# Optimization experiments

Measured on AMD Instinct MI355X. Metric: run time of the kernel, lower is better.

The kernel has to match this reference:

```python
import jax, jax.numpy as jnp
import numpy as np

N_HEADS = 16

def setup_inputs() -> dict:
    key = jax.random.key(0)
    ks = jax.random.split(key, 7)
    B, S, D = 2, 2048, 1024
    sc = 1.0 / np.sqrt(D)
    return {
        "x": jax.random.normal(ks[0], (B, S, D), dtype=jnp.float32),
        "Wq": jax.random.normal(ks[1], (D, D), dtype=jnp.float32) * sc,
        "bq": jax.random.normal(ks[2], (D,), dtype=jnp.float32) * 0.02,
        "Wk": jax.random.normal(ks[3], (D, D), dtype=jnp.float32) * sc,
        "bk": jax.random.normal(ks[4], (D,), dtype=jnp.float32) * 0.02,
        "Wv": jax.random.normal(ks[5], (D, D), dtype=jnp.float32) * sc,
        "bv": jax.random.normal(ks[6], (D,), dtype=jnp.float32) * 0.02,
    }

def reference(x, Wq, bq, Wk, bk, Wv, bv):
    B, S, D = x.shape
    H = N_HEADS
    W = D // H  # head width
    # QKV projections (torch Linear: x @ W^T + b); here weights stored as [D_in, D_out]
    q = x @ Wq + bq
    k = x @ Wk + bk
    v = x @ Wv + bv
    # split last dim into heads -> [B, H, S, W]
    q = q.reshape(B, S, H, W).transpose(0, 2, 1, 3)
    k = k.reshape(B, S, H, W).transpose(0, 2, 1, 3)
    v = v.reshape(B, S, H, W).transpose(0, 2, 1, 3)
    # scaled dot-product attention; full [B,H,S,S] scores as in original
    scores = jnp.einsum("bhqw,bhkw->bhqk", q, k) / jnp.sqrt(jnp.asarray(W, x.dtype))
    probs = jax.nn.softmax(scores, axis=-1)  # dropout is identity in eval mode
    h = jnp.einsum("bhqk,bhkw->bhqw", probs, v)
    # merge heads -> [B, S, D]
    return h.transpose(0, 2, 1, 3).reshape(B, S, D)
```

## Files before the change

### kernel.cpp

```cpp
#include <hip/hip_runtime.h>

typedef _Float16 H16;
typedef _Float16 half8 __attribute__((ext_vector_type(8)));
typedef _Float16 half4 __attribute__((ext_vector_type(4)));
typedef float f32x4 __attribute__((ext_vector_type(4)));

constexpr int Bb = 2, S = 2048, D = 1024, NH = 16, HW = 64;
constexpr int M = Bb * S;

constexpr size_t XH_OFF = 0;
constexpr size_t WT_OFF = XH_OFF + (size_t)M * D * 2;
constexpr size_t Q_OFF  = WT_OFF + 3ull * D * D * 2;
constexpr size_t K_OFF  = Q_OFF + (size_t)M * D * 2;
constexpr size_t VT_OFF = K_OFF + (size_t)M * D * 2;

#define GLOAD_LDS16(g, l)                                        \
  __builtin_amdgcn_global_load_lds(                              \
      (const __attribute__((address_space(1))) void*)(g),        \
      (__attribute__((address_space(3))) void*)(l), 16, 0, 0)

__global__ __launch_bounds__(256) void cvt_x(const float* __restrict__ x,
                                             H16* __restrict__ xh) {
  size_t i = ((size_t)blockIdx.x * 256 + threadIdx.x) * 8;
  float4 a = *(const float4*)(x + i);
  float4 b = *(const float4*)(x + i + 4);
  half8 h = {(H16)a.x, (H16)a.y, (H16)a.z, (H16)a.w,
             (H16)b.x, (H16)b.y, (H16)b.z, (H16)b.w};
  *(half8*)(xh + i) = h;
}

__global__ __launch_bounds__(256) void wt_cvt(const float* __restrict__ w0,
                                              const float* __restrict__ w1,
                                              const float* __restrict__ w2,
                                              H16* __restrict__ wt) {
  __shared__ H16 tile[64][65];
  const float* w = blockIdx.z == 0 ? w0 : blockIdx.z == 1 ? w1 : w2;
  H16* out = wt + (size_t)blockIdx.z * D * D;
  int t = threadIdx.x;
  int c = t & 63, r4 = t >> 6;
  int bx = blockIdx.x * 64, by = blockIdx.y * 64;
#pragma unroll 4
  for (int it = 0; it < 16; ++it) {
    int row = it * 4 + r4;
    tile[c][row] = (H16)w[(size_t)(by + row) * D + bx + c];
  }
  __syncthreads();
#pragma unroll 4
  for (int it = 0; it < 16; ++it) {
    int row = it * 4 + r4;
    out[(size_t)(bx + row) * D + by + c] = tile[row][c];
  }
}

__global__ __launch_bounds__(256) void qkv_gemm(
    const H16* __restrict__ xh, const H16* __restrict__ wt,
    const float* __restrict__ bq, const float* __restrict__ bk,
    const float* __restrict__ bv, H16* __restrict__ qo, H16* __restrict__ ko,
    H16* __restrict__ vto) {
  __shared__ __align__(16) H16 As[128 * 32];
  __shared__ __align__(16) H16 Bs[128 * 32];
  const int z = blockIdx.z;
  const H16* w = wt + (size_t)z * D * D;
  const float* bias = z == 0 ? bq : z == 1 ? bk : bv;
  const int bm = blockIdx.y * 128, bn = blockIdx.x * 128;
  const int t = threadIdx.x;
  const int wave = t >> 6, lane = t & 63;
  const int g = lane >> 4, c = lane & 15;
  const int wm = (wave >> 1) * 64, wn = (wave & 1) * 64;

  f32x4 acc[4][4] = {};

  for (int kk = 0; kk < D; kk += 32) {
#pragma unroll
    for (int rnd = 0; rnd < 2; ++rnd) {
      int cid = rnd * 256 + t;
      int row = cid >> 2, k0 = (cid & 3) * 8;
      GLOAD_LDS16(&xh[(size_t)(bm + row) * D + kk + k0], &As[cid * 8]);
      GLOAD_LDS16(&w[(size_t)(bn + row) * D + kk + k0], &Bs[cid * 8]);
    }
    __syncthreads();
    half8 af[4], bf[4];
#pragma unroll
    for (int i = 0; i < 4; ++i) {
      af[i] = *(const half8*)&As[(wm + i * 16 + c) * 32 + g * 8];
      bf[i] = *(const half8*)&Bs[(wn + i * 16 + c) * 32 + g * 8];
    }
#pragma unroll
    for (int i = 0; i < 4; ++i)
#pragma unroll
      for (int j = 0; j < 4; ++j)
        acc[i][j] =
            __builtin_amdgcn_mfma_f32_16x16x32_f16(af[i], bf[j], acc[i][j], 0, 0, 0);
    __syncthreads();
  }

#pragma unroll
  for (int i = 0; i < 4; ++i) {
#pragma unroll
    for (int j = 0; j < 4; ++j) {
      int coln = bn + wn + j * 16 + c;
      float bse = bias[coln];
      int h = coln >> 6, wcol = coln & 63;
#pragma unroll
      for (int r = 0; r < 4; ++r) {
        int row = bm + wm + i * 16 + g * 4 + r;
        float val = acc[i][j][r] + bse;
        int bbx = row >> 11, s = row & (S - 1);
        size_t bh = (size_t)(bbx * NH + h);
        if (z == 0)
          qo[(bh * S + s) * HW + wcol] = (H16)val;
        else if (z == 1)
          ko[(bh * S + s) * HW + wcol] = (H16)val;
        else
          vto[(bh * HW + wcol) * S + s] = (H16)val;
      }
    }
  }
}

__global__ __launch_bounds__(256, 3) void attn(const H16* __restrict__ q,
                                               const H16* __restrict__ k,
                                               const H16* __restrict__ vt,
                                               float* __restrict__ out) {
  constexpr int PSTR = 72;
  __shared__ __align__(16) H16 Ks[2][64 * 64];
  __shared__ __align__(16) H16 Vs[2][64 * 64];
  __shared__ __align__(16) H16 pl[4][16 * PSTR];

  const int id = blockIdx.x;
  const int xcd = id & 7, slot = id >> 3;
  const int bh = xcd * 4 + (slot >> 5);
  const int qt = slot & 31;

  const int t = threadIdx.x, wave = t >> 6, lane = t & 63;
  const int g = lane >> 4, c = lane & 15;
  const int q0 = qt * 64 + wave * 16;
  const H16* qp = q + ((size_t)bh * S + q0) * HW;
  const H16* kp = k + (size_t)bh * S * HW;
  const H16* vp = vt + (size_t)bh * HW * S;

  const int r0 = t >> 3, k8a = t & 7;
  const int r1 = (t + 256) >> 3, k8b = t & 7;
  const int wsw0 = r0 * 64 + ((k8a ^ (r0 & 7)) * 8);
  const int wsw1 = r1 * 64 + ((k8b ^ (r1 & 7)) * 8);

  half8 qb0 = *(const half8*)&qp[c * HW + g * 8];
  half8 qb1 = *(const half8*)&qp[c * HW + 32 + g * 8];

  f32x4 o[4] = {};
  float mx = -__builtin_inff(), l = 0.f;
  const float sc = 0.125f * 1.44269504088896f;
  H16* myp = pl[wave];

  const int sw0 = (g ^ (c & 7)) * 8;
  const int sw1 = ((4 + g) ^ (c & 7)) * 8;

  {
    half8 ka = *(const half8*)&kp[(size_t)r0 * HW + k8a * 8];
    half8 kb = *(const half8*)&kp[(size_t)r1 * HW + k8b * 8];
    half8 va = *(const half8*)&vp[(size_t)r0 * S + k8a * 8];
    half8 vb = *(const half8*)&vp[(size_t)r1 * S + k8b * 8];
    *(half8*)&Ks[0][wsw0] = ka;
    *(half8*)&Ks[0][wsw1] = kb;
    *(half8*)&Vs[0][wsw0] = va;
    *(half8*)&Vs[0][wsw1] = vb;
  }

  int buf = 0;
  for (int it = 0; it < S / 64; ++it) {
    __syncthreads();

    half8 nka, nkb, nva, nvb;
    if (it + 1 < S / 64) {
      const int nck = (it + 1) * 64;
      nka = *(const half8*)&kp[(size_t)(nck + r0) * HW + k8a * 8];
      nkb = *(const half8*)&kp[(size_t)(nck + r1) * HW + k8b * 8];
      nva = *(const half8*)&vp[(size_t)r0 * S + nck + k8a * 8];
      nvb = *(const half8*)&vp[(size_t)r1 * S + nck + k8b * 8];
    }

    const H16* ks = Ks[buf];
    const H16* vs = Vs[buf];

    f32x4 st[4];
#pragma unroll
    for (int kt = 0; kt < 4; ++kt) {
      const H16* kr = &ks[(kt * 16 + c) * 64];
      half8 ka0 = *(const half8*)&kr[sw0];
      half8 ka1 = *(const half8*)&kr[sw1];
      f32x4 z = {};
      st[kt] = __builtin_amdgcn_mfma_f32_16x16x32_f16(ka0, qb0, z, 0, 0, 0);
      st[kt] = __builtin_amdgcn_mfma_f32_16x16x32_f16(ka1, qb1, st[kt], 0, 0, 0);
    }

    float cm = st[0][0];
#pragma unroll
    for (int kt = 0; kt < 4; ++kt)
#pragma unroll
      for (int r = 0; r < 4; ++r) cm = fmaxf(cm, st[kt][r]);
    cm = fmaxf(cm, __shfl_xor(cm, 16, 64));
    cm = fmaxf(cm, __shfl_xor(cm, 32, 64));
    float mn = fmaxf(mx, cm);
    float alpha = __builtin_amdgcn_exp2f((mx - mn) * sc);
    mx = mn;
    float msc = mn * sc;

    float p[4][4];
    float rs = 0.f;
#pragma unroll
    for (int kt = 0; kt < 4; ++kt)
#pragma unroll
      for (int r = 0; r < 4; ++r) {
        p[kt][r] = __builtin_amdgcn_exp2f(st[kt][r] * sc - msc);
        rs += p[kt][r];
      }
    rs += __shfl_xor(rs, 16, 64);
    rs += __shfl_xor(rs, 32, 64);
    l = l * alpha + rs;

#pragma unroll
    for (int wt = 0; wt < 4; ++wt)
#pragma unroll
      for (int r = 0; r < 4; ++r) o[wt][r] *= alpha;

#pragma unroll
    for (int kt = 0; kt < 4; ++kt) {
      half4 pk = {(H16)p[kt][0], (H16)p[kt][1], (H16)p[kt][2], (H16)p[kt][3]};
      *(half4*)&myp[c * PSTR + kt * 16 + g * 4] = pk;
    }
    half8 pb0 = *(const half8*)&myp[c * PSTR + g * 8];
    half8 pb1 = *(const half8*)&myp[c * PSTR + 32 + g * 8];

#pragma unroll
    for (int wt = 0; wt < 4; ++wt) {
      const H16* vr = &vs[(wt * 16 + c) * 64];
      half8 va0 = *(const half8*)&vr[sw0];
      half8 va1 = *(const half8*)&vr[sw1];
      o[wt] = __builtin_amdgcn_mfma_f32_16x16x32_f16(va0, pb0, o[wt], 0, 0, 0);
      o[wt] = __builtin_amdgcn_mfma_f32_16x16x32_f16(va1, pb1, o[wt], 0, 0, 0);
    }

    if (it + 1 < S / 64) {
      H16* kd = Ks[buf ^ 1];
      H16* vd = Vs[buf ^ 1];
      *(half8*)&kd[wsw0] = nka;
      *(half8*)&kd[wsw1] = nkb;
      *(half8*)&vd[wsw0] = nva;
      *(half8*)&vd[wsw1] = nvb;
    }
    buf ^= 1;
  }

  const float inv = 1.0f / l;
  const int bbx = bh >> 4, h = bh & 15;
  float* orow = out + ((size_t)bbx * S + q0 + c) * D + h * HW;
#pragma unroll
  for (int wt = 0; wt < 4; ++wt) {
    float4 v4 = {o[wt][0] * inv, o[wt][1] * inv, o[wt][2] * inv, o[wt][3] * inv};
    *(float4*)&orow[wt * 16 + g * 4] = v4;
  }
}

extern "C" void kernel_launch(void* const* d_in, const int* in_sizes, int n_in,
                              void* d_out, int out_size, void* d_ws,
                              size_t ws_size, hipStream_t stream) {
  const float* x = (const float*)d_in[0];
  const float* Wq = (const float*)d_in[1];
  const float* bq = (const float*)d_in[2];
  const float* Wk = (const float*)d_in[3];
  const float* bk = (const float*)d_in[4];
  const float* Wv = (const float*)d_in[5];
  const float* bv = (const float*)d_in[6];
  float* out = (float*)d_out;
  char* ws = (char*)d_ws;
  H16* xh = (H16*)(ws + XH_OFF);
  H16* wt = (H16*)(ws + WT_OFF);
  H16* qw = (H16*)(ws + Q_OFF);
  H16* kw = (H16*)(ws + K_OFF);
  H16* vtw = (H16*)(ws + VT_OFF);

  cvt_x<<<dim3((M * D) / (256 * 8)), 256, 0, stream>>>(x, xh);
  wt_cvt<<<dim3(16, 16, 3), 256, 0, stream>>>(Wq, Wk, Wv, wt);
  qkv_gemm<<<dim3(8, 32, 3), 256, 0, stream>>>(xh, wt, bq, bk, bv, qw, kw, vtw);
  attn<<<dim3(1024), 256, 0, stream>>>(qw, kw, vtw, out);
}
```

Measured before the change: 190.5 us.

## Process 32 query rows per wave to reuse K/V tiles across two query groups

Each wave now handles two 16-row query groups (128 queries per block) instead of one, so every K/V tile loaded into shared memory and every K/V fragment read from it feeds twice as many MFMAs. The grid is halved to 512 blocks, which cuts total global K/V traffic and LDS reads per unit of work. In exchange, register use per thread roughly doubles for accumulators and scores, which may lower occupancy. With 512 blocks over 256 CUs there are also fewer waves available to hide latency.

```diff
diff --git a/kernel.cpp b/kernel.cpp
--- a/kernel.cpp
+++ b/kernel.cpp
@@ -125,30 +125,35 @@
   constexpr int PSTR = 72;
   __shared__ __align__(16) H16 Ks[2][64 * 64];
   __shared__ __align__(16) H16 Vs[2][64 * 64];
-  __shared__ __align__(16) H16 pl[4][16 * PSTR];
+  __shared__ __align__(16) H16 pl[4][32 * PSTR];
 
   const int id = blockIdx.x;
   const int xcd = id & 7, slot = id >> 3;
-  const int bh = xcd * 4 + (slot >> 5);
-  const int qt = slot & 31;
+  const int bh = xcd * 4 + (slot >> 4);
+  const int qt = slot & 15;
 
   const int t = threadIdx.x, wave = t >> 6, lane = t & 63;
   const int g = lane >> 4, c = lane & 15;
-  const int q0 = qt * 64 + wave * 16;
+  const int q0 = qt * 128 + wave * 32;
   const H16* qp = q + ((size_t)bh * S + q0) * HW;
   const H16* kp = k + (size_t)bh * S * HW;
   const H16* vp = vt + (size_t)bh * HW * S;
 
-  const int r0 = t >> 3, k8a = t & 7;
-  const int r1 = (t + 256) >> 3, k8b = t & 7;
-  const int wsw0 = r0 * 64 + ((k8a ^ (r0 & 7)) * 8);
-  const int wsw1 = r1 * 64 + ((k8b ^ (r1 & 7)) * 8);
-
-  half8 qb0 = *(const half8*)&qp[c * HW + g * 8];
-  half8 qb1 = *(const half8*)&qp[c * HW + 32 + g * 8];
-
-  f32x4 o[4] = {};
-  float mx = -__builtin_inff(), l = 0.f;
+  const int r0 = t >> 3, k8 = t & 7;
+  const int r1 = r0 + 32;
+  const int wsw0 = r0 * 64 + ((k8 ^ (r0 & 7)) * 8);
+  const int wsw1 = r1 * 64 + ((k8 ^ (r1 & 7)) * 8);
+
+  half8 qb[2][2];
+#pragma unroll
+  for (int qg = 0; qg < 2; ++qg) {
+    qb[qg][0] = *(const half8*)&qp[(qg * 16 + c) * HW + g * 8];
+    qb[qg][1] = *(const half8*)&qp[(qg * 16 + c) * HW + 32 + g * 8];
+  }
+
+  f32x4 o[4][2] = {};
+  float mx[2] = {-__builtin_inff(), -__builtin_inff()};
+  float l[2] = {0.f, 0.f};
   const float sc = 0.125f * 1.44269504088896f;
   H16* myp = pl[wave];
 
@@ -156,10 +161,10 @@
   const int sw1 = ((4 + g) ^ (c & 7)) * 8;
 
   {
-    half8 ka = *(const half8*)&kp[(size_t)r0 * HW + k8a * 8];
-    half8 kb = *(const half8*)&kp[(size_t)r1 * HW + k8b * 8];
-    half8 va = *(const half8*)&vp[(size_t)r0 * S + k8a * 8];
-    half8 vb = *(const half8*)&vp[(size_t)r1 * S + k8b * 8];
+    half8 ka = *(const half8*)&kp[(size_t)r0 * HW + k8 * 8];
+    half8 kb = *(const half8*)&kp[(size_t)r1 * HW + k8 * 8];
+    half8 va = *(const half8*)&vp[(size_t)r0 * S + k8 * 8];
+    half8 vb = *(const half8*)&vp[(size_t)r1 * S + k8 * 8];
     *(half8*)&Ks[0][wsw0] = ka;
     *(half8*)&Ks[0][wsw1] = kb;
     *(half8*)&Vs[0][wsw0] = va;
@@ -173,71 +178,85 @@
     half8 nka, nkb, nva, nvb;
     if (it + 1 < S / 64) {
       const int nck = (it + 1) * 64;
-      nka = *(const half8*)&kp[(size_t)(nck + r0) * HW + k8a * 8];
-      nkb = *(const half8*)&kp[(size_t)(nck + r1) * HW + k8b * 8];
-      nva = *(const half8*)&vp[(size_t)r0 * S + nck + k8a * 8];
-      nvb = *(const half8*)&vp[(size_t)r1 * S + nck + k8b * 8];
+      nka = *(const half8*)&kp[(size_t)(nck + r0) * HW + k8 * 8];
+      nkb = *(const half8*)&kp[(size_t)(nck + r1) * HW + k8 * 8];
+      nva = *(const half8*)&vp[(size_t)r0 * S + nck + k8 * 8];
+      nvb = *(const half8*)&vp[(size_t)r1 * S + nck + k8 * 8];
     }
 
     const H16* ks = Ks[buf];
     const H16* vs = Vs[buf];
 
-    f32x4 st[4];
+    f32x4 st[4][2];
 #pragma unroll
     for (int kt = 0; kt < 4; ++kt) {
       const H16* kr = &ks[(kt * 16 + c) * 64];
       half8 ka0 = *(const half8*)&kr[sw0];
       half8 ka1 = *(const half8*)&kr[sw1];
-      f32x4 z = {};
-      st[kt] = __builtin_amdgcn_mfma_f32_16x16x32_f16(ka0, qb0, z, 0, 0, 0);
-      st[kt] = __builtin_amdgcn_mfma_f32_16x16x32_f16(ka1, qb1, st[kt], 0, 0, 0);
-    }
-
-    float cm = st[0][0];
-#pragma unroll
-    for (int kt = 0; kt < 4; ++kt)
-#pragma unroll
-      for (int r = 0; r < 4; ++r) cm = fmaxf(cm, st[kt][r]);
-    cm = fmaxf(cm, __shfl_xor(cm, 16, 64));
-    cm = fmaxf(cm, __shfl_xor(cm, 32, 64));
-    float mn = fmaxf(mx, cm);
-    float alpha = __builtin_amdgcn_exp2f((mx - mn) * sc);
-    mx = mn;
-    float msc = mn * sc;
-
-    float p[4][4];
-    float rs = 0.f;
-#pragma unroll
-    for (int kt = 0; kt < 4; ++kt)
-#pragma unroll
-      for (int r = 0; r < 4; ++r) {
-        p[kt][r] = __builtin_amdgcn_exp2f(st[kt][r] * sc - msc);
-        rs += p[kt][r];
+#pragma unroll
+      for (int qg = 0; qg < 2; ++qg) {
+        f32x4 z = {};
+        st[kt][qg] =
+            __builtin_amdgcn_mfma_f32_16x16x32_f16(ka0, qb[qg][0], z, 0, 0, 0);
+        st[kt][qg] = __builtin_amdgcn_mfma_f32_16x16x32_f16(ka1, qb[qg][1],
+                                                            st[kt][qg], 0, 0, 0);
       }
-    rs += __shfl_xor(rs, 16, 64);
-    rs += __shfl_xor(rs, 32, 64);
-    l = l * alpha + rs;
-
-#pragma unroll
-    for (int wt = 0; wt < 4; ++wt)
-#pragma unroll
-      for (int r = 0; r < 4; ++r) o[wt][r] *= alpha;
-
-#pragma unroll
-    for (int kt = 0; kt < 4; ++kt) {
-      half4 pk = {(H16)p[kt][0], (H16)p[kt][1], (H16)p[kt][2], (H16)p[kt][3]};
-      *(half4*)&myp[c * PSTR + kt * 16 + g * 4] = pk;
-    }
-    half8 pb0 = *(const half8*)&myp[c * PSTR + g * 8];
-    half8 pb1 = *(const half8*)&myp[c * PSTR + 32 + g * 8];
+    }
+
+    half8 pb[2][2];
+#pragma unroll
+    for (int qg = 0; qg < 2; ++qg) {
+      float cm = st[0][qg][0];
+#pragma unroll
+      for (int kt = 0; kt < 4; ++kt)
+#pragma unroll
+        for (int r = 0; r < 4; ++r) cm = fmaxf(cm, st[kt][qg][r]);
+      cm = fmaxf(cm, __shfl_xor(cm, 16, 64));
+      cm = fmaxf(cm, __shfl_xor(cm, 32, 64));
+      float mn = fmaxf(mx[qg], cm);
+      float alpha = __builtin_amdgcn_exp2f((mx[qg] - mn) * sc);
+      mx[qg] = mn;
+      float msc = mn * sc;
+
+      float p[4][4];
+      float rs = 0.f;
+#pragma unroll
+      for (int kt = 0; kt < 4; ++kt)
+#pragma unroll
+        for (int r = 0; r < 4; ++r) {
+          p[kt][r] = __builtin_amdgcn_exp2f(st[kt][qg][r] * sc - msc);
+          rs += p[kt][r];
+        }
+      rs += __shfl_xor(rs, 16, 64);
+      rs += __shfl_xor(rs, 32, 64);
+      l[qg] = l[qg] * alpha + rs;
+
+#pragma unroll
+      for (int wt = 0; wt < 4; ++wt)
+#pragma unroll
+        for (int r = 0; r < 4; ++r) o[wt][qg][r] *= alpha;
+
+#pragma unroll
+      for (int kt = 0; kt < 4; ++kt) {
+        half4 pk = {(H16)p[kt][0], (H16)p[kt][1], (H16)p[kt][2], (H16)p[kt][3]};
+        *(half4*)&myp[(qg * 16 + c) * PSTR + kt * 16 + g * 4] = pk;
+      }
+      pb[qg][0] = *(const half8*)&myp[(qg * 16 + c) * PSTR + g * 8];
+      pb[qg][1] = *(const half8*)&myp[(qg * 16 + c) * PSTR + 32 + g * 8];
+    }
 
 #pragma unroll
     for (int wt = 0; wt < 4; ++wt) {
       const H16* vr = &vs[(wt * 16 + c) * 64];
       half8 va0 = *(const half8*)&vr[sw0];
       half8 va1 = *(const half8*)&vr[sw1];
-      o[wt] = __builtin_amdgcn_mfma_f32_16x16x32_f16(va0, pb0, o[wt], 0, 0, 0);
-      o[wt] = __builtin_amdgcn_mfma_f32_16x16x32_f16(va1, pb1, o[wt], 0, 0, 0);
+#pragma unroll
+      for (int qg = 0; qg < 2; ++qg) {
+        o[wt][qg] = __builtin_amdgcn_mfma_f32_16x16x32_f16(va0, pb[qg][0],
+                                                           o[wt][qg], 0, 0, 0);
+        o[wt][qg] = __builtin_amdgcn_mfma_f32_16x16x32_f16(va1, pb[qg][1],
+                                                           o[wt][qg], 0, 0, 0);
+      }
     }
 
     if (it + 1 < S / 64) {
@@ -251,13 +270,17 @@
     buf ^= 1;
   }
 
-  const float inv = 1.0f / l;
   const int bbx = bh >> 4, h = bh & 15;
-  float* orow = out + ((size_t)bbx * S + q0 + c) * D + h * HW;
-#pragma unroll
-  for (int wt = 0; wt < 4; ++wt) {
-    float4 v4 = {o[wt][0] * inv, o[wt][1] * inv, o[wt][2] * inv, o[wt][3] * inv};
-    *(float4*)&orow[wt * 16 + g * 4] = v4;
+#pragma unroll
+  for (int qg = 0; qg < 2; ++qg) {
+    const float inv = 1.0f / l[qg];
+    float* orow = out + ((size_t)bbx * S + q0 + qg * 16 + c) * D + h * HW;
+#pragma unroll
+    for (int wt = 0; wt < 4; ++wt) {
+      float4 v4 = {o[wt][qg][0] * inv, o[wt][qg][1] * inv, o[wt][qg][2] * inv,
+                   o[wt][qg][3] * inv};
+      *(float4*)&orow[wt * 16 + g * 4] = v4;
+    }
   }
 }
 
@@ -282,5 +305,5 @@
   cvt_x<<<dim3((M * D) / (256 * 8)), 256, 0, stream>>>(x, xh);
   wt_cvt<<<dim3(16, 16, 3), 256, 0, stream>>>(Wq, Wk, Wv, wt);
   qkv_gemm<<<dim3(8, 32, 3), 256, 0, stream>>>(xh, wt, bq, bk, bv, qw, kw, vtw);
-  attn<<<dim3(1024), 256, 0, stream>>>(qw, kw, vtw, out);
-}
+  attn<<<dim3(512), 256, 0, stream>>>(qw, kw, vtw, out);
+}
```

New measurement: 183.4 us. 1.04x faster.
